# Kernel optimization log

Measured on AMD Instinct MI355X. Metric: run time of the kernel, lower is better.

The kernel has to match this reference:

```python
import jax, jax.numpy as jnp
import numpy as np

RNN = 64      # rnn_hidden_dim
HID = 64      # hidden_dim
ENC = 3       # encoder_dim
NAG = 8       # n_agents
NACT = 14     # n_actions
CLIP = 0.2    # args.exp_clip (variance floor)
BN_EPS = 1e-5


def _bn(x, g, b):
    # BatchNorm1d in training mode: batch stats, biased variance
    m = x.mean(0)
    v = jnp.mean((x - m) ** 2, 0)
    return g * (x - m) * jax.lax.rsqrt(v + BN_EPS) + b


def setup_inputs() -> dict:
    key = jax.random.key(0)
    ks = jax.random.split(key, 16)
    B, INP = 8192, 96

    def w(k, shape, fan):
        return (jax.random.normal(k, shape, jnp.float32) / np.float32(np.sqrt(fan)))

    d = {}
    d["inputs"] = jax.random.normal(ks[0], (B * NAG, INP), jnp.float32)
    d["hidden_state"] = jax.random.normal(ks[1], (B * NAG, RNN), jnp.float32)
    d["noise"] = jax.random.normal(ks[2], (B, NAG, NAG * ENC), jnp.float32)
    d["fc1_w"] = w(ks[3], (INP, RNN), INP); d["fc1_b"] = jnp.zeros((RNN,), jnp.float32)
    d["w_ih"] = w(ks[4], (RNN, 3 * RNN), RNN); d["w_hh"] = w(ks[5], (RNN, 3 * RNN), RNN)
    d["b_ih"] = jnp.zeros((3 * RNN,), jnp.float32); d["b_hh"] = jnp.zeros((3 * RNN,), jnp.float32)
    d["aw1_w"] = w(ks[6], (RNN, HID), RNN); d["aw1_b"] = jnp.zeros((HID,), jnp.float32)
    d["aw_g"] = jnp.ones((HID,), jnp.float32); d["aw_be"] = jnp.zeros((HID,), jnp.float32)
    d["aw2_w"] = w(ks[7], (HID, 2 * NAG * ENC), HID); d["aw2_b"] = jnp.zeros((2 * NAG * ENC,), jnp.float32)
    d["po1_w"] = w(ks[8], (2 * RNN, HID), 2 * RNN); d["po1_b"] = jnp.zeros((HID,), jnp.float32)
    d["po_g"] = jnp.ones((HID,), jnp.float32); d["po_be"] = jnp.zeros((HID,), jnp.float32)
    d["po2_w"] = w(ks[9], (HID, 2 * ENC), HID); d["po2_b"] = jnp.zeros((2 * ENC,), jnp.float32)
    d["fc2_w"] = w(ks[10], (RNN + ENC * NAG, NACT), RNN + ENC * NAG); d["fc2_b"] = jnp.zeros((NACT,), jnp.float32)
    return d


def reference(inputs, hidden_state, noise,
              fc1_w, fc1_b, w_ih, w_hh, b_ih, b_hh,
              aw1_w, aw1_b, aw_g, aw_be, aw2_w, aw2_b,
              po1_w, po1_b, po_g, po_be, po2_w, po2_b,
              fc2_w, fc2_b):
    B, n, enc = noise.shape[0], NAG, ENC

    x = jax.nn.relu(inputs @ fc1_w + fc1_b)                      # [B*n, RNN]
    h_in = hidden_state.reshape(-1, RNN)

    # torch GRUCell
    gi = x @ w_ih + b_ih
    gh = h_in @ w_hh + b_hh
    ir, iz, i_n = jnp.split(gi, 3, axis=-1)
    hr, hz, h_n = jnp.split(gh, 3, axis=-1)
    r = jax.nn.sigmoid(ir + hr)
    z = jax.nn.sigmoid(iz + hz)
    nt = jnp.tanh(i_n + r * h_n)
    h = (1.0 - z) * nt + z * h_in                                # [B*n, RNN]

    # awareness encoder
    a = jax.nn.relu(_bn(h @ aw1_w + aw1_b, aw_g, aw_be))
    aw = (a @ aw2_w + aw2_b).reshape(B, n, 2 * n * enc)
    mu = aw[:, :, : n * enc]
    sigma = jnp.maximum(jnp.exp(aw[:, :, n * enc:]), CLIP)       # variance
    c = (mu + jnp.sqrt(sigma) * noise).reshape(-1, n * enc)      # rsample

    x_out = jnp.concatenate([h, c], axis=-1) @ fc2_w + fc2_b     # [B*n, NACT]

    # poster branch (training mode): all-pairs concat H[b, j, id] = [h[b,id], h[b,j]]
    hd = jax.lax.stop_gradient(h).reshape(B, n, RNN)
    Hi = jnp.broadcast_to(hd[:, None, :, :], (B, n, n, RNN))     # axis2 = id
    Hj = jnp.broadcast_to(hd[:, :, None, :], (B, n, n, RNN))     # axis1 = j
    H = jnp.concatenate([Hi, Hj], axis=-1).reshape(-1, 2 * RNN)  # [B*n*n, 2*RNN]

    p = jax.nn.relu(_bn(H @ po1_w + po1_b, po_g, po_be))
    out = (p @ po2_w + po2_b).reshape(B, n, 2 * n * enc)
    mu1 = out[:, :, : n * enc]
    sigma1 = jnp.maximum(jnp.exp(out[:, :, n * enc:]), CLIP)

    # KL between diagonal Gaussians (sigma, sigma1 are variances)
    kl = 0.5 * (jnp.log(sigma1 / sigma) + (sigma + (mu - mu1) ** 2) / sigma1 - 1.0)
    KL = kl.mean(axis=-1).mean(axis=-1, keepdims=True)           # [B, 1]
    return (x_out, h, KL)
```

## Files before the change

kernel.cpp:

```cpp
#include <hip/hip_runtime.h>
#include <math.h>

#define NROWS 65536
#define NB    8192
#define STAT_OFF  0
#define WPACK_OFF 448
#define OUT_XOUT 0
#define OUT_H    917504
#define OUT_KL   5111808

typedef __attribute__((ext_vector_type(8))) short bhalf8;
typedef __attribute__((ext_vector_type(4))) float floatx4;
typedef __attribute__((ext_vector_type(4))) unsigned short u16x4;

__device__ __forceinline__ float sigmf(float x) { return 1.0f / (1.0f + __expf(-x)); }
__device__ __forceinline__ float tanhfast(float x) {
    x = fminf(fmaxf(x, -15.f), 15.f);
    float e = __expf(-2.f * x);
    return (1.f - e) / (1.f + e);
}
__device__ __forceinline__ unsigned short f2bf(float f) {
    unsigned int u = __float_as_uint(f);
    u += 0x7FFFu + ((u >> 16) & 1u);
    return (unsigned short)(u >> 16);
}
__device__ __forceinline__ float bf2f(unsigned short s) {
    return __uint_as_float(((unsigned int)s) << 16);
}
__device__ __forceinline__ bhalf8 pack8(float4 a, float4 b) {
    bhalf8 r;
    r[0] = (short)f2bf(a.x); r[1] = (short)f2bf(a.y);
    r[2] = (short)f2bf(a.z); r[3] = (short)f2bf(a.w);
    r[4] = (short)f2bf(b.x); r[5] = (short)f2bf(b.y);
    r[6] = (short)f2bf(b.z); r[7] = (short)f2bf(b.w);
    return r;
}

__global__ void k_prep(const float* __restrict__ fc1_w,
                       const float* __restrict__ w_ih, const float* __restrict__ w_hh,
                       const float* __restrict__ aw1_w, const float* __restrict__ po1_w,
                       const float* __restrict__ aw2_w, const float* __restrict__ fc2_w,
                       float* __restrict__ ws)
{
    const int t = threadIdx.x;
    if (blockIdx.x == 0)
        for (int i = t; i < 448; i += 256) ws[STAT_OFF + i] = 0.f;

    unsigned short* wpk = (unsigned short*)(ws + WPACK_OFF);
    for (int f = blockIdx.x * 256 + t; f < 5952; f += gridDim.x * 256) {
        int lane, c, tile;
        const float* src;
        int colbase, krowstride, kofs = 0, kmax = 1 << 30, colmax = 16;
        if (f < 768) {
            tile = f / 192; c = (f % 192) / 64; lane = f % 64;
            src = fc1_w; krowstride = 64; colbase = tile * 16;
        } else if (f < 3840) {
            int f2 = f - 768;
            tile = f2 / 128; c = (f2 % 128) / 64; lane = f2 % 64;
            if (tile < 12) { src = w_ih; colbase = tile * 16; }
            else           { src = w_hh; colbase = (tile - 12) * 16; }
            krowstride = 192;
        } else if (f < 5376) {
            int f3 = f - 3840;
            tile = f3 / 128; c = (f3 % 128) / 64; lane = f3 % 64;
            if (tile < 4)       { src = aw1_w; colbase = tile * 16; }
            else if (tile < 8)  { src = po1_w; colbase = (tile - 4) * 16; }
            else                { src = po1_w; colbase = (tile - 8) * 16; kofs = 64; }
            krowstride = 64;
        } else if (f < 5760) {
            int f4 = f - 5376;
            tile = f4 / 128; c = (f4 % 128) / 64; lane = f4 % 64;
            src = aw2_w; krowstride = 48; colbase = tile * 16;
        } else {
            int f5 = f - 5760;
            c = f5 / 64; lane = f5 % 64;
            src = fc2_w; krowstride = 14; colbase = 0;
            kmax = 88; colmax = 14;
        }
        int n = lane & 15, quad = lane >> 4;
        int col = colbase + n;
        unsigned short o[8];
        #pragma unroll
        for (int j = 0; j < 8; j++) {
            int k = c * 32 + quad * 8 + j + kofs;
            float v = (k < kmax && n < colmax) ? src[(size_t)k * krowstride + col] : 0.f;
            o[j] = f2bf(v);
        }
        u16x4 lo, hi;
        lo.x = o[0]; lo.y = o[1]; lo.z = o[2]; lo.w = o[3];
        hi.x = o[4]; hi.y = o[5]; hi.z = o[6]; hi.w = o[7];
        *(u16x4*)&wpk[f * 8]     = lo;
        *(u16x4*)&wpk[f * 8 + 4] = hi;
    }
}

__global__ __launch_bounds__(256, 4) void k_front(
    const float* __restrict__ inp, const float* __restrict__ hin,
    const float* __restrict__ fc1_b,
    const float* __restrict__ b_ih, const float* __restrict__ b_hh,
    const float* __restrict__ aw1_b,
    float* __restrict__ h_out, float* __restrict__ ws)
{
    __shared__ __align__(16) unsigned short s_xb[128 * 80];
    __shared__ float s_stat[448];

    const int t = threadIdx.x;
    const int row0 = blockIdx.x * 128;
    const int lane = t & 63;
    const int w = t >> 6;
    const int n16 = lane & 15;
    const int quad = lane >> 4;

    for (int i = t; i < 448; i += 256) s_stat[i] = 0.f;
    __syncthreads();

    const bhalf8* wp1 = (const bhalf8*)((const unsigned short*)(ws + WPACK_OFF));
    const bhalf8* wp2 = wp1 + 768;
    const bhalf8* wp3 = wp1 + 3840;

    bhalf8 ai[2][3], ahf[2][2];
    #pragma unroll
    for (int u = 0; u < 2; u++) {
        const float* gi = inp + (size_t)(row0 + w * 32 + u * 16 + n16) * 96 + quad * 8;
        #pragma unroll
        for (int kc = 0; kc < 3; kc++)
            ai[u][kc] = pack8(*(const float4*)&gi[kc * 32], *(const float4*)&gi[kc * 32 + 4]);
        const float* gh = hin + (size_t)(row0 + w * 32 + u * 16 + n16) * 64 + quad * 8;
        #pragma unroll
        for (int kc = 0; kc < 2; kc++)
            ahf[u][kc] = pack8(*(const float4*)&gh[kc * 32], *(const float4*)&gh[kc * 32 + 4]);
    }

    #pragma unroll
    for (int g = 0; g < 4; g++) {
        bhalf8 f0 = wp1[(g * 3 + 0) * 64 + lane];
        bhalf8 f1 = wp1[(g * 3 + 1) * 64 + lane];
        bhalf8 f2 = wp1[(g * 3 + 2) * 64 + lane];
        int col = g * 16 + n16;
        float bb = fc1_b[col];
        #pragma unroll
        for (int u = 0; u < 2; u++) {
            floatx4 d = {0.f, 0.f, 0.f, 0.f};
            d = __builtin_amdgcn_mfma_f32_16x16x32_bf16(ai[u][0], f0, d, 0, 0, 0);
            d = __builtin_amdgcn_mfma_f32_16x16x32_bf16(ai[u][1], f1, d, 0, 0, 0);
            d = __builtin_amdgcn_mfma_f32_16x16x32_bf16(ai[u][2], f2, d, 0, 0, 0);
            #pragma unroll
            for (int q = 0; q < 4; q++)
                s_xb[(w * 32 + u * 16 + quad * 4 + q) * 80 + col] = f2bf(fmaxf(d[q] + bb, 0.f));
        }
    }
    bhalf8 ax[2][2];
    #pragma unroll
    for (int u = 0; u < 2; u++) {
        int mr = w * 32 + u * 16 + n16;
        ax[u][0] = *(const bhalf8*)&s_xb[mr * 80 + 0  + quad * 8];
        ax[u][1] = *(const bhalf8*)&s_xb[mr * 80 + 32 + quad * 8];
    }

    #pragma unroll
    for (int g = 0; g < 4; g++) {
        int col = g * 16 + n16;
        floatx4 dr[2], dz[2], dn[2], dh[2];
        {
            bhalf8 f0 = wp2[((0 + g) * 2 + 0) * 64 + lane];
            bhalf8 f1 = wp2[((0 + g) * 2 + 1) * 64 + lane];
            bhalf8 f2 = wp2[((12 + g) * 2 + 0) * 64 + lane];
            bhalf8 f3 = wp2[((12 + g) * 2 + 1) * 64 + lane];
            #pragma unroll
            for (int u = 0; u < 2; u++) {
                floatx4 d = {0.f, 0.f, 0.f, 0.f};
                d = __builtin_amdgcn_mfma_f32_16x16x32_bf16(ax[u][0], f0, d, 0, 0, 0);
                d = __builtin_amdgcn_mfma_f32_16x16x32_bf16(ax[u][1], f1, d, 0, 0, 0);
                d = __builtin_amdgcn_mfma_f32_16x16x32_bf16(ahf[u][0], f2, d, 0, 0, 0);
                d = __builtin_amdgcn_mfma_f32_16x16x32_bf16(ahf[u][1], f3, d, 0, 0, 0);
                dr[u] = d;
            }
        }
        {
            bhalf8 f0 = wp2[((4 + g) * 2 + 0) * 64 + lane];
            bhalf8 f1 = wp2[((4 + g) * 2 + 1) * 64 + lane];
            bhalf8 f2 = wp2[((16 + g) * 2 + 0) * 64 + lane];
            bhalf8 f3 = wp2[((16 + g) * 2 + 1) * 64 + lane];
            #pragma unroll
            for (int u = 0; u < 2; u++) {
                floatx4 d = {0.f, 0.f, 0.f, 0.f};
                d = __builtin_amdgcn_mfma_f32_16x16x32_bf16(ax[u][0], f0, d, 0, 0, 0);
                d = __builtin_amdgcn_mfma_f32_16x16x32_bf16(ax[u][1], f1, d, 0, 0, 0);
                d = __builtin_amdgcn_mfma_f32_16x16x32_bf16(ahf[u][0], f2, d, 0, 0, 0);
                d = __builtin_amdgcn_mfma_f32_16x16x32_bf16(ahf[u][1], f3, d, 0, 0, 0);
                dz[u] = d;
            }
        }
        {
            bhalf8 f0 = wp2[((8 + g) * 2 + 0) * 64 + lane];
            bhalf8 f1 = wp2[((8 + g) * 2 + 1) * 64 + lane];
            #pragma unroll
            for (int u = 0; u < 2; u++) {
                floatx4 d = {0.f, 0.f, 0.f, 0.f};
                d = __builtin_amdgcn_mfma_f32_16x16x32_bf16(ax[u][0], f0, d, 0, 0, 0);
                d = __builtin_amdgcn_mfma_f32_16x16x32_bf16(ax[u][1], f1, d, 0, 0, 0);
                dn[u] = d;
            }
        }
        {
            bhalf8 f0 = wp2[((20 + g) * 2 + 0) * 64 + lane];
            bhalf8 f1 = wp2[((20 + g) * 2 + 1) * 64 + lane];
            #pragma unroll
            for (int u = 0; u < 2; u++) {
                floatx4 d = {0.f, 0.f, 0.f, 0.f};
                d = __builtin_amdgcn_mfma_f32_16x16x32_bf16(ahf[u][0], f0, d, 0, 0, 0);
                d = __builtin_amdgcn_mfma_f32_16x16x32_bf16(ahf[u][1], f1, d, 0, 0, 0);
                dh[u] = d;
            }
        }
        float br_ = b_ih[col] + b_hh[col];
        float bz_ = b_ih[64 + col] + b_hh[64 + col];
        float bin_ = b_ih[128 + col];
        float bhn_ = b_hh[128 + col];
        #pragma unroll
        for (int u = 0; u < 2; u++) {
            #pragma unroll
            for (int q = 0; q < 4; q++) {
                int lrow = w * 32 + u * 16 + quad * 4 + q;
                size_t grow = (size_t)(row0 + lrow);
                float r  = sigmf(dr[u][q] + br_);
                float z  = sigmf(dz[u][q] + bz_);
                float nt = tanhfast(dn[u][q] + bin_ + r * (dh[u][q] + bhn_));
                float hp = hin[grow * 64 + col];
                float h  = (1.f - z) * nt + z * hp;
                h_out[grow * 64 + col] = h;
                s_xb[lrow * 80 + col] = f2bf(h);
            }
        }
    }

    bhalf8 hh[2][2];
    #pragma unroll
    for (int u = 0; u < 2; u++) {
        int mr = w * 32 + u * 16 + n16;
        hh[u][0] = *(const bhalf8*)&s_xb[mr * 80 + 0  + quad * 8];
        hh[u][1] = *(const bhalf8*)&s_xb[mr * 80 + 32 + quad * 8];
    }

    #pragma unroll
    for (int g = 0; g < 4; g++) {
        int col = g * 16 + n16;
        floatx4 da[2], du[2], dvv[2];
        {
            bhalf8 f0 = wp3[(g * 2 + 0) * 64 + lane];
            bhalf8 f1 = wp3[(g * 2 + 1) * 64 + lane];
            #pragma unroll
            for (int u = 0; u < 2; u++) {
                floatx4 d = {0.f, 0.f, 0.f, 0.f};
                d = __builtin_amdgcn_mfma_f32_16x16x32_bf16(hh[u][0], f0, d, 0, 0, 0);
                d = __builtin_amdgcn_mfma_f32_16x16x32_bf16(hh[u][1], f1, d, 0, 0, 0);
                da[u] = d;
            }
        }
        {
            bhalf8 f0 = wp3[((4 + g) * 2 + 0) * 64 + lane];
            bhalf8 f1 = wp3[((4 + g) * 2 + 1) * 64 + lane];
            #pragma unroll
            for (int u = 0; u < 2; u++) {
                floatx4 d = {0.f, 0.f, 0.f, 0.f};
                d = __builtin_amdgcn_mfma_f32_16x16x32_bf16(hh[u][0], f0, d, 0, 0, 0);
                d = __builtin_amdgcn_mfma_f32_16x16x32_bf16(hh[u][1], f1, d, 0, 0, 0);
                du[u] = d;
            }
        }
        {
            bhalf8 f0 = wp3[((8 + g) * 2 + 0) * 64 + lane];
            bhalf8 f1 = wp3[((8 + g) * 2 + 1) * 64 + lane];
            #pragma unroll
            for (int u = 0; u < 2; u++) {
                floatx4 d = {0.f, 0.f, 0.f, 0.f};
                d = __builtin_amdgcn_mfma_f32_16x16x32_bf16(hh[u][0], f0, d, 0, 0, 0);
                d = __builtin_amdgcn_mfma_f32_16x16x32_bf16(hh[u][1], f1, d, 0, 0, 0);
                dvv[u] = d;
            }
        }
        float ab = aw1_b[col];
        float s1 = 0.f, s2 = 0.f, suq = 0.f, svq = 0.f;
        float su[2] = {0.f, 0.f}, sv[2] = {0.f, 0.f};
        #pragma unroll
        for (int u = 0; u < 2; u++) {
            #pragma unroll
            for (int q = 0; q < 4; q++) {
                float a = da[u][q] + ab; s1 += a; s2 += a * a;
                float uv = du[u][q]; su[u] += uv; suq += uv * uv;
                float vv = dvv[u][q]; sv[u] += vv; svq += vv * vv;
            }
        }
        #pragma unroll
        for (int u = 0; u < 2; u++) {
            float u8 = su[u] + __shfl_xor(su[u], 16, 64);
            float v8 = sv[u] + __shfl_xor(sv[u], 16, 64);
            if ((quad & 1) == 0)
                atomicAdd(&s_stat[384 + col], u8 * v8 * (1.f / 64.f));
        }
        float sut = su[0] + su[1];
        float svt = sv[0] + sv[1];
        float t1 = s1 + __shfl_xor(s1, 16, 64);   t1 += __shfl_xor(t1, 32, 64);
        float t2 = s2 + __shfl_xor(s2, 16, 64);   t2 += __shfl_xor(t2, 32, 64);
        float t3 = sut + __shfl_xor(sut, 16, 64); t3 += __shfl_xor(t3, 32, 64);
        float t4 = suq + __shfl_xor(suq, 16, 64); t4 += __shfl_xor(t4, 32, 64);
        float t5 = svt + __shfl_xor(svt, 16, 64); t5 += __shfl_xor(t5, 32, 64);
        float t6 = svq + __shfl_xor(svq, 16, 64); t6 += __shfl_xor(t6, 32, 64);
        if (quad == 0) {
            atomicAdd(&s_stat[col], t1);
            atomicAdd(&s_stat[64 + col], t2);
            atomicAdd(&s_stat[128 + col], t3);
            atomicAdd(&s_stat[192 + col], t4);
            atomicAdd(&s_stat[256 + col], t5);
            atomicAdd(&s_stat[320 + col], t6);
        }
    }
    __syncthreads();
    if (t < 64) {
        float* gs = ws + STAT_OFF;
        #pragma unroll
        for (int q = 0; q < 7; q++)
            atomicAdd(&gs[q * 64 + t], s_stat[q * 64 + t]);
    }
}

__global__ __launch_bounds__(128) void k_heads(
    const float* __restrict__ h_glob, const float* __restrict__ noise,
    const float* __restrict__ aw1_b, const float* __restrict__ aw2_b,
    const float* __restrict__ fc2_b, const float* __restrict__ po2_b,
    const float* __restrict__ aw_g, const float* __restrict__ aw_be,
    const float* __restrict__ po_g, const float* __restrict__ po_be,
    const float* __restrict__ po1_b, const float* __restrict__ po2_w,
    const float* __restrict__ ws, float* __restrict__ out)
{
    __shared__ __align__(16) unsigned short s_hb[32 * 104];
    __shared__ __align__(16) unsigned short s_Ub[32 * 80];
    __shared__ __align__(16) unsigned short s_Vb[32 * 80];
    __shared__ float s_ms[32 * 48];
    __shared__ __align__(16) float s_out[32 * 48];
    __shared__ __align__(16) float s_dv[640];
    __shared__ float s_kl[32];

    const int t = threadIdx.x;
    const int row0 = blockIdx.x * 32;
    const int b0 = blockIdx.x * 4;
    const int lane = t & 63;
    const int w = t >> 6;
    const int n16 = lane & 15;
    const int quad = lane >> 4;
    const int mrow = w * 16 + n16;

    if (t < 64) {
        const float* st = ws + STAT_OFF;
        const float invN = 1.f / 65536.f;
        float am = st[t] * invN;
        float av = st[64 + t] * invN - am * am;
        float asc = aw_g[t] * rsqrtf(av + 1e-5f);
        s_dv[t] = asc;
        s_dv[64 + t] = aw_be[t] - asc * am;
        float Eu = st[128 + t] * invN;
        float vu = st[192 + t] * invN - Eu * Eu;
        float Ev = st[256 + t] * invN;
        float vv = st[320 + t] * invN - Ev * Ev;
        float cov = st[384 + t] * (1.f / 8192.f) - Eu * Ev;
        float my = Eu + Ev + po1_b[t];
        float vy = vu + vv + 2.f * cov;
        float psc = po_g[t] * rsqrtf(vy + 1e-5f);
        s_dv[128 + t] = psc;
        s_dv[192 + t] = po_be[t] + psc * (po1_b[t] - my);
    }
    for (int i = t; i < 384; i += 128) {
        int d = i >> 6, c = i & 63;
        s_dv[256 + i] = po2_w[c * 6 + d];
    }

    {
        const float* gh = h_glob + (size_t)row0 * 64;
        for (int i = t; i < 512; i += 128) {
            int r = i >> 4, c4 = (i & 15) * 4;
            float4 v = *(const float4*)&gh[r * 64 + c4];
            u16x4 p; p.x = f2bf(v.x); p.y = f2bf(v.y); p.z = f2bf(v.z); p.w = f2bf(v.w);
            *(u16x4*)&s_hb[r * 104 + c4] = p;
        }
        for (int i = t; i < 64; i += 128) {
            int r = i >> 1, c4 = 88 + (i & 1) * 4;
            u16x4 z; z.x = 0; z.y = 0; z.z = 0; z.w = 0;
            *(u16x4*)&s_hb[r * 104 + c4] = z;
        }
    }
    __syncthreads();

    const bhalf8* wp3  = ((const bhalf8*)((const unsigned short*)(ws + WPACK_OFF))) + 3840;
    const bhalf8* wpa2 = wp3 + 1536;
    const bhalf8* wpf2 = wpa2 + 384;
    unsigned short* s_ab = (unsigned short*)s_out;

    {
        bhalf8 ah0 = *(const bhalf8*)&s_hb[mrow * 104 + 0  + quad * 8];
        bhalf8 ah1 = *(const bhalf8*)&s_hb[mrow * 104 + 32 + quad * 8];
        #pragma unroll
        for (int g = 0; g < 4; g++) {
            int col = g * 16 + n16;
            floatx4 da = {0.f, 0.f, 0.f, 0.f}, duu = {0.f, 0.f, 0.f, 0.f}, dvv = {0.f, 0.f, 0.f, 0.f};
            da  = __builtin_amdgcn_mfma_f32_16x16x32_bf16(ah0, wp3[(g * 2 + 0) * 64 + lane], da, 0, 0, 0);
            da  = __builtin_amdgcn_mfma_f32_16x16x32_bf16(ah1, wp3[(g * 2 + 1) * 64 + lane], da, 0, 0, 0);
            duu = __builtin_amdgcn_mfma_f32_16x16x32_bf16(ah0, wp3[((4 + g) * 2 + 0) * 64 + lane], duu, 0, 0, 0);
            duu = __builtin_amdgcn_mfma_f32_16x16x32_bf16(ah1, wp3[((4 + g) * 2 + 1) * 64 + lane], duu, 0, 0, 0);
            dvv = __builtin_amdgcn_mfma_f32_16x16x32_bf16(ah0, wp3[((8 + g) * 2 + 0) * 64 + lane], dvv, 0, 0, 0);
            dvv = __builtin_amdgcn_mfma_f32_16x16x32_bf16(ah1, wp3[((8 + g) * 2 + 1) * 64 + lane], dvv, 0, 0, 0);
            float ab = aw1_b[col];
            float asc = s_dv[col], ash = s_dv[64 + col];
            float psc = s_dv[128 + col], psh = s_dv[192 + col];
            #pragma unroll
            for (int q = 0; q < 4; q++) {
                int lrow = w * 16 + quad * 4 + q;
                s_ab[lrow * 80 + col] = f2bf(fmaxf(asc * (da[q] + ab) + ash, 0.f));
                s_Ub[lrow * 80 + col] = f2bf(psc * duu[q]);
                s_Vb[lrow * 80 + col] = f2bf(psc * dvv[q] + psh);
            }
        }
    }

    {
        bhalf8 aa0 = *(const bhalf8*)&s_ab[mrow * 80 + 0  + quad * 8];
        bhalf8 aa1 = *(const bhalf8*)&s_ab[mrow * 80 + 32 + quad * 8];
        #pragma unroll
        for (int g = 0; g < 3; g++) {
            floatx4 d = {0.f, 0.f, 0.f, 0.f};
            d = __builtin_amdgcn_mfma_f32_16x16x32_bf16(aa0, wpa2[(g * 2 + 0) * 64 + lane], d, 0, 0, 0);
            d = __builtin_amdgcn_mfma_f32_16x16x32_bf16(aa1, wpa2[(g * 2 + 1) * 64 + lane], d, 0, 0, 0);
            int col = g * 16 + n16;
            float bb = aw2_b[col];
            #pragma unroll
            for (int q = 0; q < 4; q++) {
                int lrow = w * 16 + quad * 4 + q;
                float v = d[q] + bb;
                s_ms[lrow * 48 + col] = (col < 24) ? v : fmaxf(__expf(v), 0.2f);
            }
        }
    }
    __syncthreads();

    for (int i = t; i < 768; i += 128) {
        int r = i / 24, m = i - r * 24;
        float c = s_ms[r * 48 + m] + sqrtf(s_ms[r * 48 + 24 + m]) * noise[(size_t)(row0 + r) * 24 + m];
        s_hb[r * 104 + 64 + m] = f2bf(c);
    }
    __syncthreads();

    {
        bhalf8 hc0 = *(const bhalf8*)&s_hb[mrow * 104 + 0  + quad * 8];
        bhalf8 hc1 = *(const bhalf8*)&s_hb[mrow * 104 + 32 + quad * 8];
        bhalf8 hc2 = *(const bhalf8*)&s_hb[mrow * 104 + 64 + quad * 8];
        floatx4 d = {0.f, 0.f, 0.f, 0.f};
        d = __builtin_amdgcn_mfma_f32_16x16x32_bf16(hc0, wpf2[0 * 64 + lane], d, 0, 0, 0);
        d = __builtin_amdgcn_mfma_f32_16x16x32_bf16(hc1, wpf2[1 * 64 + lane], d, 0, 0, 0);
        d = __builtin_amdgcn_mfma_f32_16x16x32_bf16(hc2, wpf2[2 * 64 + lane], d, 0, 0, 0);
        if (n16 < 14) {
            float bb = fc2_b[n16];
            float* xout = out + OUT_XOUT;
            #pragma unroll
            for (int q = 0; q < 4; q++) {
                size_t grow = (size_t)(row0 + w * 16 + quad * 4 + q);
                xout[grow * 14 + n16] = d[q] + bb;
            }
        }
    }
    __syncthreads();

    {
        const float* p2t = s_dv + 256;
        const int bl = t >> 5;
        const int rem = t & 31;
        const int i_ = rem >> 2;
        const int j0 = (rem & 3) * 2;
        float acc[2][6];
        #pragma unroll
        for (int jj = 0; jj < 2; jj++)
            #pragma unroll
            for (int d = 0; d < 6; d++) acc[jj][d] = 0.f;

        for (int c = 0; c < 64; c += 4) {
            u16x4 vb4 = *(const u16x4*)&s_Vb[(bl * 8 + i_) * 80 + c];
            float vv[4] = {bf2f(vb4.x), bf2f(vb4.y), bf2f(vb4.z), bf2f(vb4.w)};
            float wv[6][4];
            #pragma unroll
            for (int d = 0; d < 6; d++) *(float4*)wv[d] = *(const float4*)&p2t[d * 64 + c];
            #pragma unroll
            for (int jj = 0; jj < 2; jj++) {
                u16x4 ub4 = *(const u16x4*)&s_Ub[(bl * 8 + j0 + jj) * 80 + c];
                float p[4];
                p[0] = fmaxf(bf2f(ub4.x) + vv[0], 0.f);
                p[1] = fmaxf(bf2f(ub4.y) + vv[1], 0.f);
                p[2] = fmaxf(bf2f(ub4.z) + vv[2], 0.f);
                p[3] = fmaxf(bf2f(ub4.w) + vv[3], 0.f);
                #pragma unroll
                for (int d = 0; d < 6; d++)
                    acc[jj][d] += p[0] * wv[d][0] + p[1] * wv[d][1] + p[2] * wv[d][2] + p[3] * wv[d][3];
            }
        }
        #pragma unroll
        for (int jj = 0; jj < 2; jj++)
            #pragma unroll
            for (int d = 0; d < 6; d++)
                s_out[(bl * 8 + i_) * 48 + (j0 + jj) * 6 + d] = acc[jj][d] + po2_b[d];
    }
    __syncthreads();

    if (t < 32) {
        float s = 0.f;
        #pragma unroll 4
        for (int m = 0; m < 24; m++) {
            float mu0 = s_ms[t * 48 + m];
            float sg0 = s_ms[t * 48 + 24 + m];
            float mu1 = s_out[t * 48 + m];
            float sg1 = fmaxf(__expf(s_out[t * 48 + 24 + m]), 0.2f);
            float d0 = mu0 - mu1;
            s += __logf(sg1 / sg0) + (sg0 + d0 * d0) / sg1 - 1.f;
        }
        s_kl[t] = s;
    }
    __syncthreads();
    if (t < 4) {
        float s = 0.f;
        #pragma unroll
        for (int i = 0; i < 8; i++) s += s_kl[t * 8 + i];
        out[OUT_KL + b0 + t] = s * (0.5f / 192.f);
    }
}

extern "C" void kernel_launch(void* const* d_in, const int* in_sizes, int n_in,
                              void* d_out, int out_size, void* d_ws, size_t ws_size,
                              hipStream_t stream)
{
    (void)in_sizes; (void)n_in; (void)out_size; (void)ws_size;
    const float* inp   = (const float*)d_in[0];
    const float* hin   = (const float*)d_in[1];
    const float* noise = (const float*)d_in[2];
    const float* fc1_w = (const float*)d_in[3];
    const float* fc1_b = (const float*)d_in[4];
    const float* w_ih  = (const float*)d_in[5];
    const float* w_hh  = (const float*)d_in[6];
    const float* b_ih  = (const float*)d_in[7];
    const float* b_hh  = (const float*)d_in[8];
    const float* aw1_w = (const float*)d_in[9];
    const float* aw1_b = (const float*)d_in[10];
    const float* aw_g  = (const float*)d_in[11];
    const float* aw_be = (const float*)d_in[12];
    const float* aw2_w = (const float*)d_in[13];
    const float* aw2_b = (const float*)d_in[14];
    const float* po1_w = (const float*)d_in[15];
    const float* po1_b = (const float*)d_in[16];
    const float* po_g  = (const float*)d_in[17];
    const float* po_be = (const float*)d_in[18];
    const float* po2_w = (const float*)d_in[19];
    const float* po2_b = (const float*)d_in[20];
    const float* fc2_w = (const float*)d_in[21];
    const float* fc2_b = (const float*)d_in[22];
    float* out = (float*)d_out;
    float* ws  = (float*)d_ws;

    hipLaunchKernelGGL(k_prep,  dim3(24),   dim3(256), 0, stream,
                       fc1_w, w_ih, w_hh, aw1_w, po1_w, aw2_w, fc2_w, ws);
    hipLaunchKernelGGL(k_front, dim3(512),  dim3(256), 0, stream,
                       inp, hin, fc1_b, b_ih, b_hh, aw1_b, out + OUT_H, ws);
    hipLaunchKernelGGL(k_heads, dim3(2048), dim3(128), 0, stream,
                       out + OUT_H, noise, aw1_b, aw2_b, fc2_b, po2_b,
                       aw_g, aw_be, po_g, po_be, po1_b, po2_w, ws, out);
}
```

Measured before the change: 197.2 us.

## Halve front-kernel row tile and widen heads block to 256 threads

k_front now processes 64 rows per block instead of 128, giving one 16-row MFMA tile per wave and twice as many blocks, which lowers register pressure and raises occupancy. k_heads moves to 256 threads, with only the first two waves doing the MFMA stages while all threads share the elementwise and pairwise posterior work. The pairwise loop now gives each thread one (i,j) pair and reads the po2 weight transpose from a workspace precomputed in k_prep rather than rebuilding it in shared memory per block. The cost is idle waves during the MFMA phases, more per-block atomics for the BN statistics, and global rather than LDS reads of the po2 weights.

```diff
diff --git a/kernel.cpp b/kernel.cpp
--- a/kernel.cpp
+++ b/kernel.cpp
@@ -4,7 +4,8 @@
 #define NROWS 65536
 #define NB    8192
 #define STAT_OFF  0
-#define WPACK_OFF 448
+#define P2T_OFF   448
+#define WPACK_OFF 832
 #define OUT_XOUT 0
 #define OUT_H    917504
 #define OUT_KL   5111808
@@ -40,11 +41,17 @@
                        const float* __restrict__ w_ih, const float* __restrict__ w_hh,
                        const float* __restrict__ aw1_w, const float* __restrict__ po1_w,
                        const float* __restrict__ aw2_w, const float* __restrict__ fc2_w,
+                       const float* __restrict__ po2_w,
                        float* __restrict__ ws)
 {
     const int t = threadIdx.x;
-    if (blockIdx.x == 0)
+    if (blockIdx.x == 0) {
         for (int i = t; i < 448; i += 256) ws[STAT_OFF + i] = 0.f;
+        for (int i = t; i < 384; i += 256) {
+            int d = i >> 6, c = i & 63;
+            ws[P2T_OFF + i] = po2_w[c * 6 + d];
+        }
+    }
 
     unsigned short* wpk = (unsigned short*)(ws + WPACK_OFF);
     for (int f = blockIdx.x * 256 + t; f < 5952; f += gridDim.x * 256) {
@@ -101,15 +108,16 @@
     const float* __restrict__ aw1_b,
     float* __restrict__ h_out, float* __restrict__ ws)
 {
-    __shared__ __align__(16) unsigned short s_xb[128 * 80];
+    __shared__ __align__(16) unsigned short s_xb[64 * 80];
     __shared__ float s_stat[448];
 
     const int t = threadIdx.x;
-    const int row0 = blockIdx.x * 128;
+    const int row0 = blockIdx.x * 64;
     const int lane = t & 63;
     const int w = t >> 6;
     const int n16 = lane & 15;
     const int quad = lane >> 4;
+    const int mrow = w * 16 + n16;
 
     for (int i = t; i < 448; i += 256) s_stat[i] = 0.f;
     __syncthreads();
@@ -118,193 +126,99 @@
     const bhalf8* wp2 = wp1 + 768;
     const bhalf8* wp3 = wp1 + 3840;
 
-    bhalf8 ai[2][3], ahf[2][2];
-    #pragma unroll
-    for (int u = 0; u < 2; u++) {
-        const float* gi = inp + (size_t)(row0 + w * 32 + u * 16 + n16) * 96 + quad * 8;
+    bhalf8 ai[3], ahf[2];
+    {
+        const float* gi = inp + (size_t)(row0 + mrow) * 96 + quad * 8;
         #pragma unroll
         for (int kc = 0; kc < 3; kc++)
-            ai[u][kc] = pack8(*(const float4*)&gi[kc * 32], *(const float4*)&gi[kc * 32 + 4]);
-        const float* gh = hin + (size_t)(row0 + w * 32 + u * 16 + n16) * 64 + quad * 8;
+            ai[kc] = pack8(*(const float4*)&gi[kc * 32], *(const float4*)&gi[kc * 32 + 4]);
+        const float* gh = hin + (size_t)(row0 + mrow) * 64 + quad * 8;
         #pragma unroll
         for (int kc = 0; kc < 2; kc++)
-            ahf[u][kc] = pack8(*(const float4*)&gh[kc * 32], *(const float4*)&gh[kc * 32 + 4]);
-    }
-
-    #pragma unroll
-    for (int g = 0; g < 4; g++) {
-        bhalf8 f0 = wp1[(g * 3 + 0) * 64 + lane];
-        bhalf8 f1 = wp1[(g * 3 + 1) * 64 + lane];
-        bhalf8 f2 = wp1[(g * 3 + 2) * 64 + lane];
-        int col = g * 16 + n16;
-        float bb = fc1_b[col];
-        #pragma unroll
-        for (int u = 0; u < 2; u++) {
-            floatx4 d = {0.f, 0.f, 0.f, 0.f};
-            d = __builtin_amdgcn_mfma_f32_16x16x32_bf16(ai[u][0], f0, d, 0, 0, 0);
-            d = __builtin_amdgcn_mfma_f32_16x16x32_bf16(ai[u][1], f1, d, 0, 0, 0);
-            d = __builtin_amdgcn_mfma_f32_16x16x32_bf16(ai[u][2], f2, d, 0, 0, 0);
-            #pragma unroll
-            for (int q = 0; q < 4; q++)
-                s_xb[(w * 32 + u * 16 + quad * 4 + q) * 80 + col] = f2bf(fmaxf(d[q] + bb, 0.f));
-        }
-    }
-    bhalf8 ax[2][2];
-    #pragma unroll
-    for (int u = 0; u < 2; u++) {
-        int mr = w * 32 + u * 16 + n16;
-        ax[u][0] = *(const bhalf8*)&s_xb[mr * 80 + 0  + quad * 8];
-        ax[u][1] = *(const bhalf8*)&s_xb[mr * 80 + 32 + quad * 8];
+            ahf[kc] = pack8(*(const float4*)&gh[kc * 32], *(const float4*)&gh[kc * 32 + 4]);
     }
 
     #pragma unroll
     for (int g = 0; g < 4; g++) {
         int col = g * 16 + n16;
-        floatx4 dr[2], dz[2], dn[2], dh[2];
-        {
-            bhalf8 f0 = wp2[((0 + g) * 2 + 0) * 64 + lane];
-            bhalf8 f1 = wp2[((0 + g) * 2 + 1) * 64 + lane];
-            bhalf8 f2 = wp2[((12 + g) * 2 + 0) * 64 + lane];
-            bhalf8 f3 = wp2[((12 + g) * 2 + 1) * 64 + lane];
-            #pragma unroll
-            for (int u = 0; u < 2; u++) {
-                floatx4 d = {0.f, 0.f, 0.f, 0.f};
-                d = __builtin_amdgcn_mfma_f32_16x16x32_bf16(ax[u][0], f0, d, 0, 0, 0);
-                d = __builtin_amdgcn_mfma_f32_16x16x32_bf16(ax[u][1], f1, d, 0, 0, 0);
-                d = __builtin_amdgcn_mfma_f32_16x16x32_bf16(ahf[u][0], f2, d, 0, 0, 0);
-                d = __builtin_amdgcn_mfma_f32_16x16x32_bf16(ahf[u][1], f3, d, 0, 0, 0);
-                dr[u] = d;
-            }
-        }
-        {
-            bhalf8 f0 = wp2[((4 + g) * 2 + 0) * 64 + lane];
-            bhalf8 f1 = wp2[((4 + g) * 2 + 1) * 64 + lane];
-            bhalf8 f2 = wp2[((16 + g) * 2 + 0) * 64 + lane];
-            bhalf8 f3 = wp2[((16 + g) * 2 + 1) * 64 + lane];
-            #pragma unroll
-            for (int u = 0; u < 2; u++) {
-                floatx4 d = {0.f, 0.f, 0.f, 0.f};
-                d = __builtin_amdgcn_mfma_f32_16x16x32_bf16(ax[u][0], f0, d, 0, 0, 0);
-                d = __builtin_amdgcn_mfma_f32_16x16x32_bf16(ax[u][1], f1, d, 0, 0, 0);
-                d = __builtin_amdgcn_mfma_f32_16x16x32_bf16(ahf[u][0], f2, d, 0, 0, 0);
-                d = __builtin_amdgcn_mfma_f32_16x16x32_bf16(ahf[u][1], f3, d, 0, 0, 0);
-                dz[u] = d;
-            }
-        }
-        {
-            bhalf8 f0 = wp2[((8 + g) * 2 + 0) * 64 + lane];
-            bhalf8 f1 = wp2[((8 + g) * 2 + 1) * 64 + lane];
-            #pragma unroll
-            for (int u = 0; u < 2; u++) {
-                floatx4 d = {0.f, 0.f, 0.f, 0.f};
-                d = __builtin_amdgcn_mfma_f32_16x16x32_bf16(ax[u][0], f0, d, 0, 0, 0);
-                d = __builtin_amdgcn_mfma_f32_16x16x32_bf16(ax[u][1], f1, d, 0, 0, 0);
-                dn[u] = d;
-            }
-        }
-        {
-            bhalf8 f0 = wp2[((20 + g) * 2 + 0) * 64 + lane];
-            bhalf8 f1 = wp2[((20 + g) * 2 + 1) * 64 + lane];
-            #pragma unroll
-            for (int u = 0; u < 2; u++) {
-                floatx4 d = {0.f, 0.f, 0.f, 0.f};
-                d = __builtin_amdgcn_mfma_f32_16x16x32_bf16(ahf[u][0], f0, d, 0, 0, 0);
-                d = __builtin_amdgcn_mfma_f32_16x16x32_bf16(ahf[u][1], f1, d, 0, 0, 0);
-                dh[u] = d;
-            }
-        }
+        floatx4 d = {0.f, 0.f, 0.f, 0.f};
+        d = __builtin_amdgcn_mfma_f32_16x16x32_bf16(ai[0], wp1[(g * 3 + 0) * 64 + lane], d, 0, 0, 0);
+        d = __builtin_amdgcn_mfma_f32_16x16x32_bf16(ai[1], wp1[(g * 3 + 1) * 64 + lane], d, 0, 0, 0);
+        d = __builtin_amdgcn_mfma_f32_16x16x32_bf16(ai[2], wp1[(g * 3 + 2) * 64 + lane], d, 0, 0, 0);
+        float bb = fc1_b[col];
+        #pragma unroll
+        for (int q = 0; q < 4; q++)
+            s_xb[(w * 16 + quad * 4 + q) * 80 + col] = f2bf(fmaxf(d[q] + bb, 0.f));
+    }
+    bhalf8 ax[2];
+    ax[0] = *(const bhalf8*)&s_xb[mrow * 80 + 0  + quad * 8];
+    ax[1] = *(const bhalf8*)&s_xb[mrow * 80 + 32 + quad * 8];
+
+    #pragma unroll
+    for (int g = 0; g < 4; g++) {
+        int col = g * 16 + n16;
+        floatx4 dr = {0.f, 0.f, 0.f, 0.f}, dz = {0.f, 0.f, 0.f, 0.f};
+        floatx4 dn = {0.f, 0.f, 0.f, 0.f}, dh = {0.f, 0.f, 0.f, 0.f};
+        dr = __builtin_amdgcn_mfma_f32_16x16x32_bf16(ax[0],  wp2[((0 + g) * 2 + 0) * 64 + lane], dr, 0, 0, 0);
+        dr = __builtin_amdgcn_mfma_f32_16x16x32_bf16(ax[1],  wp2[((0 + g) * 2 + 1) * 64 + lane], dr, 0, 0, 0);
+        dr = __builtin_amdgcn_mfma_f32_16x16x32_bf16(ahf[0], wp2[((12 + g) * 2 + 0) * 64 + lane], dr, 0, 0, 0);
+        dr = __builtin_amdgcn_mfma_f32_16x16x32_bf16(ahf[1], wp2[((12 + g) * 2 + 1) * 64 + lane], dr, 0, 0, 0);
+        dz = __builtin_amdgcn_mfma_f32_16x16x32_bf16(ax[0],  wp2[((4 + g) * 2 + 0) * 64 + lane], dz, 0, 0, 0);
+        dz = __builtin_amdgcn_mfma_f32_16x16x32_bf16(ax[1],  wp2[((4 + g) * 2 + 1) * 64 + lane], dz, 0, 0, 0);
+        dz = __builtin_amdgcn_mfma_f32_16x16x32_bf16(ahf[0], wp2[((16 + g) * 2 + 0) * 64 + lane], dz, 0, 0, 0);
+        dz = __builtin_amdgcn_mfma_f32_16x16x32_bf16(ahf[1], wp2[((16 + g) * 2 + 1) * 64 + lane], dz, 0, 0, 0);
+        dn = __builtin_amdgcn_mfma_f32_16x16x32_bf16(ax[0],  wp2[((8 + g) * 2 + 0) * 64 + lane], dn, 0, 0, 0);
+        dn = __builtin_amdgcn_mfma_f32_16x16x32_bf16(ax[1],  wp2[((8 + g) * 2 + 1) * 64 + lane], dn, 0, 0, 0);
+        dh = __builtin_amdgcn_mfma_f32_16x16x32_bf16(ahf[0], wp2[((20 + g) * 2 + 0) * 64 + lane], dh, 0, 0, 0);
+        dh = __builtin_amdgcn_mfma_f32_16x16x32_bf16(ahf[1], wp2[((20 + g) * 2 + 1) * 64 + lane], dh, 0, 0, 0);
         float br_ = b_ih[col] + b_hh[col];
         float bz_ = b_ih[64 + col] + b_hh[64 + col];
         float bin_ = b_ih[128 + col];
         float bhn_ = b_hh[128 + col];
         #pragma unroll
-        for (int u = 0; u < 2; u++) {
-            #pragma unroll
-            for (int q = 0; q < 4; q++) {
-                int lrow = w * 32 + u * 16 + quad * 4 + q;
-                size_t grow = (size_t)(row0 + lrow);
-                float r  = sigmf(dr[u][q] + br_);
-                float z  = sigmf(dz[u][q] + bz_);
-                float nt = tanhfast(dn[u][q] + bin_ + r * (dh[u][q] + bhn_));
-                float hp = hin[grow * 64 + col];
-                float h  = (1.f - z) * nt + z * hp;
-                h_out[grow * 64 + col] = h;
-                s_xb[lrow * 80 + col] = f2bf(h);
-            }
-        }
-    }
-
-    bhalf8 hh[2][2];
-    #pragma unroll
-    for (int u = 0; u < 2; u++) {
-        int mr = w * 32 + u * 16 + n16;
-        hh[u][0] = *(const bhalf8*)&s_xb[mr * 80 + 0  + quad * 8];
-        hh[u][1] = *(const bhalf8*)&s_xb[mr * 80 + 32 + quad * 8];
-    }
+        for (int q = 0; q < 4; q++) {
+            int lrow = w * 16 + quad * 4 + q;
+            size_t grow = (size_t)(row0 + lrow);
+            float r  = sigmf(dr[q] + br_);
+            float z  = sigmf(dz[q] + bz_);
+            float nt = tanhfast(dn[q] + bin_ + r * (dh[q] + bhn_));
+            float hp = hin[grow * 64 + col];
+            float h  = (1.f - z) * nt + z * hp;
+            h_out[grow * 64 + col] = h;
+            s_xb[lrow * 80 + col] = f2bf(h);
+        }
+    }
+
+    bhalf8 hh0 = *(const bhalf8*)&s_xb[mrow * 80 + 0  + quad * 8];
+    bhalf8 hh1 = *(const bhalf8*)&s_xb[mrow * 80 + 32 + quad * 8];
 
     #pragma unroll
     for (int g = 0; g < 4; g++) {
         int col = g * 16 + n16;
-        floatx4 da[2], du[2], dvv[2];
-        {
-            bhalf8 f0 = wp3[(g * 2 + 0) * 64 + lane];
-            bhalf8 f1 = wp3[(g * 2 + 1) * 64 + lane];
-            #pragma unroll
-            for (int u = 0; u < 2; u++) {
-                floatx4 d = {0.f, 0.f, 0.f, 0.f};
-                d = __builtin_amdgcn_mfma_f32_16x16x32_bf16(hh[u][0], f0, d, 0, 0, 0);
-                d = __builtin_amdgcn_mfma_f32_16x16x32_bf16(hh[u][1], f1, d, 0, 0, 0);
-                da[u] = d;
-            }
-        }
-        {
-            bhalf8 f0 = wp3[((4 + g) * 2 + 0) * 64 + lane];
-            bhalf8 f1 = wp3[((4 + g) * 2 + 1) * 64 + lane];
-            #pragma unroll
-            for (int u = 0; u < 2; u++) {
-                floatx4 d = {0.f, 0.f, 0.f, 0.f};
-                d = __builtin_amdgcn_mfma_f32_16x16x32_bf16(hh[u][0], f0, d, 0, 0, 0);
-                d = __builtin_amdgcn_mfma_f32_16x16x32_bf16(hh[u][1], f1, d, 0, 0, 0);
-                du[u] = d;
-            }
-        }
-        {
-            bhalf8 f0 = wp3[((8 + g) * 2 + 0) * 64 + lane];
-            bhalf8 f1 = wp3[((8 + g) * 2 + 1) * 64 + lane];
-            #pragma unroll
-            for (int u = 0; u < 2; u++) {
-                floatx4 d = {0.f, 0.f, 0.f, 0.f};
-                d = __builtin_amdgcn_mfma_f32_16x16x32_bf16(hh[u][0], f0, d, 0, 0, 0);
-                d = __builtin_amdgcn_mfma_f32_16x16x32_bf16(hh[u][1], f1, d, 0, 0, 0);
-                dvv[u] = d;
-            }
-        }
+        floatx4 da = {0.f, 0.f, 0.f, 0.f}, du = {0.f, 0.f, 0.f, 0.f}, dv = {0.f, 0.f, 0.f, 0.f};
+        da = __builtin_amdgcn_mfma_f32_16x16x32_bf16(hh0, wp3[(g * 2 + 0) * 64 + lane], da, 0, 0, 0);
+        da = __builtin_amdgcn_mfma_f32_16x16x32_bf16(hh1, wp3[(g * 2 + 1) * 64 + lane], da, 0, 0, 0);
+        du = __builtin_amdgcn_mfma_f32_16x16x32_bf16(hh0, wp3[((4 + g) * 2 + 0) * 64 + lane], du, 0, 0, 0);
+        du = __builtin_amdgcn_mfma_f32_16x16x32_bf16(hh1, wp3[((4 + g) * 2 + 1) * 64 + lane], du, 0, 0, 0);
+        dv = __builtin_amdgcn_mfma_f32_16x16x32_bf16(hh0, wp3[((8 + g) * 2 + 0) * 64 + lane], dv, 0, 0, 0);
+        dv = __builtin_amdgcn_mfma_f32_16x16x32_bf16(hh1, wp3[((8 + g) * 2 + 1) * 64 + lane], dv, 0, 0, 0);
         float ab = aw1_b[col];
-        float s1 = 0.f, s2 = 0.f, suq = 0.f, svq = 0.f;
-        float su[2] = {0.f, 0.f}, sv[2] = {0.f, 0.f};
-        #pragma unroll
-        for (int u = 0; u < 2; u++) {
-            #pragma unroll
-            for (int q = 0; q < 4; q++) {
-                float a = da[u][q] + ab; s1 += a; s2 += a * a;
-                float uv = du[u][q]; su[u] += uv; suq += uv * uv;
-                float vv = dvv[u][q]; sv[u] += vv; svq += vv * vv;
-            }
-        }
-        #pragma unroll
-        for (int u = 0; u < 2; u++) {
-            float u8 = su[u] + __shfl_xor(su[u], 16, 64);
-            float v8 = sv[u] + __shfl_xor(sv[u], 16, 64);
-            if ((quad & 1) == 0)
-                atomicAdd(&s_stat[384 + col], u8 * v8 * (1.f / 64.f));
-        }
-        float sut = su[0] + su[1];
-        float svt = sv[0] + sv[1];
+        float s1 = 0.f, s2 = 0.f, su = 0.f, suq = 0.f, sv = 0.f, svq = 0.f;
+        #pragma unroll
+        for (int q = 0; q < 4; q++) {
+            float a = da[q] + ab; s1 += a; s2 += a * a;
+            float uv = du[q]; su += uv; suq += uv * uv;
+            float vv = dv[q]; sv += vv; svq += vv * vv;
+        }
+        float u8 = su + __shfl_xor(su, 16, 64);
+        float v8 = sv + __shfl_xor(sv, 16, 64);
+        if ((quad & 1) == 0)
+            atomicAdd(&s_stat[384 + col], u8 * v8 * (1.f / 64.f));
         float t1 = s1 + __shfl_xor(s1, 16, 64);   t1 += __shfl_xor(t1, 32, 64);
         float t2 = s2 + __shfl_xor(s2, 16, 64);   t2 += __shfl_xor(t2, 32, 64);
-        float t3 = sut + __shfl_xor(sut, 16, 64); t3 += __shfl_xor(t3, 32, 64);
+        float t3 = u8 + __shfl_xor(u8, 32, 64);
         float t4 = suq + __shfl_xor(suq, 16, 64); t4 += __shfl_xor(t4, 32, 64);
-        float t5 = svt + __shfl_xor(svt, 16, 64); t5 += __shfl_xor(t5, 32, 64);
+        float t5 = v8 + __shfl_xor(v8, 32, 64);
         float t6 = svq + __shfl_xor(svq, 16, 64); t6 += __shfl_xor(t6, 32, 64);
         if (quad == 0) {
             atomicAdd(&s_stat[col], t1);
@@ -324,21 +238,21 @@
     }
 }
 
-__global__ __launch_bounds__(128) void k_heads(
+__global__ __launch_bounds__(256) void k_heads(
     const float* __restrict__ h_glob, const float* __restrict__ noise,
     const float* __restrict__ aw1_b, const float* __restrict__ aw2_b,
     const float* __restrict__ fc2_b, const float* __restrict__ po2_b,
     const float* __restrict__ aw_g, const float* __restrict__ aw_be,
     const float* __restrict__ po_g, const float* __restrict__ po_be,
-    const float* __restrict__ po1_b, const float* __restrict__ po2_w,
+    const float* __restrict__ po1_b,
     const float* __restrict__ ws, float* __restrict__ out)
 {
     __shared__ __align__(16) unsigned short s_hb[32 * 104];
     __shared__ __align__(16) unsigned short s_Ub[32 * 80];
     __shared__ __align__(16) unsigned short s_Vb[32 * 80];
     __shared__ float s_ms[32 * 48];
-    __shared__ __align__(16) float s_out[32 * 48];
-    __shared__ __align__(16) float s_dv[640];
+    __shared__ __align__(16) float s_buf[32 * 48];
+    __shared__ float s_dv[256];
     __shared__ float s_kl[32];
 
     const int t = threadIdx.x;
@@ -369,21 +283,17 @@
         s_dv[128 + t] = psc;
         s_dv[192 + t] = po_be[t] + psc * (po1_b[t] - my);
     }
-    for (int i = t; i < 384; i += 128) {
-        int d = i >> 6, c = i & 63;
-        s_dv[256 + i] = po2_w[c * 6 + d];
-    }
 
     {
         const float* gh = h_glob + (size_t)row0 * 64;
-        for (int i = t; i < 512; i += 128) {
+        for (int i = t; i < 512; i += 256) {
             int r = i >> 4, c4 = (i & 15) * 4;
             float4 v = *(const float4*)&gh[r * 64 + c4];
             u16x4 p; p.x = f2bf(v.x); p.y = f2bf(v.y); p.z = f2bf(v.z); p.w = f2bf(v.w);
             *(u16x4*)&s_hb[r * 104 + c4] = p;
         }
-        for (int i = t; i < 64; i += 128) {
-            int r = i >> 1, c4 = 88 + (i & 1) * 4;
+        if (t < 64) {
+            int r = t >> 1, c4 = 88 + (t & 1) * 4;
             u16x4 z; z.x = 0; z.y = 0; z.z = 0; z.w = 0;
             *(u16x4*)&s_hb[r * 104 + c4] = z;
         }
@@ -393,9 +303,9 @@
     const bhalf8* wp3  = ((const bhalf8*)((const unsigned short*)(ws + WPACK_OFF))) + 3840;
     const bhalf8* wpa2 = wp3 + 1536;
     const bhalf8* wpf2 = wpa2 + 384;
-    unsigned short* s_ab = (unsigned short*)s_out;
-
-    {
+    unsigned short* s_ab = (unsigned short*)s_buf;
+
+    if (w < 2) {
         bhalf8 ah0 = *(const bhalf8*)&s_hb[mrow * 104 + 0  + quad * 8];
         bhalf8 ah1 = *(const bhalf8*)&s_hb[mrow * 104 + 32 + quad * 8];
         #pragma unroll
@@ -419,9 +329,6 @@
                 s_Vb[lrow * 80 + col] = f2bf(psc * dvv[q] + psh);
             }
         }
-    }
-
-    {
         bhalf8 aa0 = *(const bhalf8*)&s_ab[mrow * 80 + 0  + quad * 8];
         bhalf8 aa1 = *(const bhalf8*)&s_ab[mrow * 80 + 32 + quad * 8];
         #pragma unroll
@@ -441,14 +348,14 @@
     }
     __syncthreads();
 
-    for (int i = t; i < 768; i += 128) {
+    for (int i = t; i < 768; i += 256) {
         int r = i / 24, m = i - r * 24;
         float c = s_ms[r * 48 + m] + sqrtf(s_ms[r * 48 + 24 + m]) * noise[(size_t)(row0 + r) * 24 + m];
         s_hb[r * 104 + 64 + m] = f2bf(c);
     }
     __syncthreads();
 
-    {
+    if (w < 2) {
         bhalf8 hc0 = *(const bhalf8*)&s_hb[mrow * 104 + 0  + quad * 8];
         bhalf8 hc1 = *(const bhalf8*)&s_hb[mrow * 104 + 32 + quad * 8];
         bhalf8 hc2 = *(const bhalf8*)&s_hb[mrow * 104 + 64 + quad * 8];
@@ -468,42 +375,34 @@
     }
     __syncthreads();
 
+    float* s_out = s_buf;
     {
-        const float* p2t = s_dv + 256;
-        const int bl = t >> 5;
-        const int rem = t & 31;
-        const int i_ = rem >> 2;
-        const int j0 = (rem & 3) * 2;
-        float acc[2][6];
-        #pragma unroll
-        for (int jj = 0; jj < 2; jj++)
+        const float* p2t = ws + P2T_OFF;
+        const int bl = t >> 6;
+        const int rem = t & 63;
+        const int i_ = rem >> 3;
+        const int j_ = rem & 7;
+        float acc[6] = {0.f, 0.f, 0.f, 0.f, 0.f, 0.f};
+        #pragma unroll
+        for (int c = 0; c < 64; c += 8) {
+            bhalf8 vb = *(const bhalf8*)&s_Vb[(bl * 8 + i_) * 80 + c];
+            bhalf8 ub = *(const bhalf8*)&s_Ub[(bl * 8 + j_) * 80 + c];
+            float p[8];
             #pragma unroll
-            for (int d = 0; d < 6; d++) acc[jj][d] = 0.f;
-
-        for (int c = 0; c < 64; c += 4) {
-            u16x4 vb4 = *(const u16x4*)&s_Vb[(bl * 8 + i_) * 80 + c];
-            float vv[4] = {bf2f(vb4.x), bf2f(vb4.y), bf2f(vb4.z), bf2f(vb4.w)};
-            float wv[6][4];
+            for (int q = 0; q < 8; q++)
+                p[q] = fmaxf(bf2f((unsigned short)ub[q]) + bf2f((unsigned short)vb[q]), 0.f);
             #pragma unroll
-            for (int d = 0; d < 6; d++) *(float4*)wv[d] = *(const float4*)&p2t[d * 64 + c];
-            #pragma unroll
-            for (int jj = 0; jj < 2; jj++) {
-                u16x4 ub4 = *(const u16x4*)&s_Ub[(bl * 8 + j0 + jj) * 80 + c];
-                float p[4];
-                p[0] = fmaxf(bf2f(ub4.x) + vv[0], 0.f);
-                p[1] = fmaxf(bf2f(ub4.y) + vv[1], 0.f);
-                p[2] = fmaxf(bf2f(ub4.z) + vv[2], 0.f);
-                p[3] = fmaxf(bf2f(ub4.w) + vv[3], 0.f);
+            for (int d = 0; d < 6; d++) {
+                const float* wd = &p2t[d * 64 + c];
+                float s = 0.f;
                 #pragma unroll
-                for (int d = 0; d < 6; d++)
-                    acc[jj][d] += p[0] * wv[d][0] + p[1] * wv[d][1] + p[2] * wv[d][2] + p[3] * wv[d][3];
+                for (int q = 0; q < 8; q++) s += p[q] * wd[q];
+                acc[d] += s;
             }
         }
         #pragma unroll
-        for (int jj = 0; jj < 2; jj++)
-            #pragma unroll
-            for (int d = 0; d < 6; d++)
-                s_out[(bl * 8 + i_) * 48 + (j0 + jj) * 6 + d] = acc[jj][d] + po2_b[d];
+        for (int d = 0; d < 6; d++)
+            s_out[(bl * 8 + i_) * 48 + j_ * 6 + d] = acc[d] + po2_b[d];
     }
     __syncthreads();
 
@@ -561,10 +460,10 @@
     float* ws  = (float*)d_ws;
 
     hipLaunchKernelGGL(k_prep,  dim3(24),   dim3(256), 0, stream,
-                       fc1_w, w_ih, w_hh, aw1_w, po1_w, aw2_w, fc2_w, ws);
-    hipLaunchKernelGGL(k_front, dim3(512),  dim3(256), 0, stream,
+                       fc1_w, w_ih, w_hh, aw1_w, po1_w, aw2_w, fc2_w, po2_w, ws);
+    hipLaunchKernelGGL(k_front, dim3(1024), dim3(256), 0, stream,
                        inp, hin, fc1_b, b_ih, b_hh, aw1_b, out + OUT_H, ws);
-    hipLaunchKernelGGL(k_heads, dim3(2048), dim3(128), 0, stream,
+    hipLaunchKernelGGL(k_heads, dim3(2048), dim3(256), 0, stream,
                        out + OUT_H, noise, aw1_b, aw2_b, fc2_b, po2_b,
-                       aw_g, aw_be, po_g, po_be, po1_b, po2_w, ws, out);
-}
+                       aw_g, aw_be, po_g, po_be, po1_b, ws, out);
+}
```

Measured after the change: 198.6 us. Within noise of the previous version (+0.7%).
